# Kernel optimization log

Measured on AMD Instinct MI355X. Metric: run time of the kernel, lower is better.

The kernel has to match this reference:

```python
import jax, jax.numpy as jnp
import numpy as np

D_BINS = 16   # piecewise-linear bins
N_PROP = 10   # hard-coded in CountModule.__init__


def pwl(w, x):
    """PiecewiseLinear.forward: w is [D_BINS+1], x any shape in [0,1]."""
    aw = jnp.abs(w)
    nw = aw / aw.sum()
    cs = jnp.cumsum(nw)               # [17] cumulative knot values
    xd = x * D_BINS
    ip = jnp.floor(xd).astype(jnp.int32)   # x >= 0 so trunc == floor
    frac = xd - ip.astype(x.dtype)
    return cs[jnp.minimum(ip, D_BINS)] + frac * nw[jnp.minimum(ip + 1, D_BINS)]


def iou(a):
    """Pairwise IoU of boxes a [B,4,n] (coords y1,x1,y2,x2) -> [B,n,n]."""
    tl = jnp.maximum(a[:, :2, :, None], a[:, :2, None, :])  # [B,2,n,n]
    br = jnp.minimum(a[:, 2:, :, None], a[:, 2:, None, :])
    wh = jnp.clip(br - tl, 0.0)
    inter = wh[:, 0] * wh[:, 1]                               # [B,n,n]
    area = jnp.clip(a[:, 2] - a[:, 0], 0.0) * jnp.clip(a[:, 3] - a[:, 1], 0.0)  # [B,n]
    return inter / (area[:, :, None] + area[:, None, :] - inter + 1e-12)


def count_forward(boxes, attention, f_weights):
    n = N_PROP
    B = boxes.shape[0]
    f = lambda i, x: pwl(f_weights[i], x)
    # keep top-n proposals by attention score
    att_v, idx = jax.lax.top_k(attention, n)                  # [B,n]
    boxes_f = jnp.take_along_axis(
        boxes, jnp.broadcast_to(idx[:, None, :], (B, 4, n)), axis=2)  # [B,4,n]
    att = jax.nn.sigmoid(att_v)
    A = att[:, :, None] * att[:, None, :]                     # outer product [B,n,n]
    Dm = 1.0 - iou(boxes_f)                                   # [B,n,n]
    A_t = f(0, A) * f(1, Dm)
    X = f(3, A) * f(4, Dm)
    # deduplicate: outer_diff on 2D att gives pairwise |a_i - a_j|; on 3D X the
    # original torch code unsqueezes both operands at the same axis, yielding zeros
    att_diff = jnp.abs(att[:, :, None] - att[:, None, :])     # [B,n,n]
    xs = X[:, :, None, :]
    score_diff = jnp.broadcast_to(jnp.abs(xs - xs), (B, n, n, n))  # zeros, as in torch
    sim = f(2, 1.0 - att_diff) * jnp.prod(f(2, 1.0 - score_diff), axis=1)  # [B,n,n]
    s_i = sim.sum(axis=2)                                     # [B,n]
    s_st = s_i[:, :, None] * s_i[:, None, :]                  # [B,n,n]
    score = A_t / s_st
    corr = f(0, att * att) / s_i
    mod_E = score.sum(axis=(1, 2))[:, None] + corr.sum(axis=1, keepdims=True)  # [B,1]
    c = jnp.sqrt(mod_E + 1e-20)
    # to_k_hot: soft two-hot over counts 0..n
    cc = jnp.clip(c, 0.0, float(n))                           # [B,1]
    ip = jnp.floor(cc).astype(jnp.int32)
    frac = cc - ip.astype(cc.dtype)
    left = jax.nn.one_hot(jnp.minimum(ip[:, 0], n), n + 1, dtype=cc.dtype)
    right = jax.nn.one_hot(jnp.minimum(ip[:, 0] + 1, n), n + 1, dtype=cc.dtype)
    o = (1.0 - frac) * left + frac * right                    # [B,n+1]
    p_a = jnp.abs(f(5, att) - 0.5)                            # [B,n]
    p_d = jnp.abs(f(6, Dm) - 0.5)                             # [B,n,n]
    gate = f(7, p_a.mean(axis=1, keepdims=True)
             + p_d.mean(axis=2).mean(axis=1, keepdims=True))  # [B,1]
    return gate * o                                           # [B,n+1]


def setup_inputs() -> dict:
    key = jax.random.key(0)
    k1, k2, k3 = jax.random.split(key, 3)
    B, M = 32768, 36
    boxes = jax.random.uniform(k1, (B, 4, M), dtype=jnp.float32)
    attention = jax.random.normal(k2, (B, M), dtype=jnp.float32)
    f_weights = jax.random.uniform(k3, (8, D_BINS + 1), dtype=jnp.float32,
                                   minval=0.25, maxval=1.75)
    return {"boxes": boxes, "attention": attention, "f_weights": f_weights}


def reference(boxes, attention, f_weights):
    return count_forward(boxes, attention, f_weights)
```

## Files before the change

kernel.cpp:

```cpp
#include <hip/hip_runtime.h>
#include <cstdint>
#include <cstddef>

#define MM 36
#define NP 10
#define BLOCK 1024
#define GPB (BLOCK / 16)
#define WPB (BLOCK / 64)

template<int CTRL>
__device__ __forceinline__ float dpp_movf(float x) {
    return __int_as_float(__builtin_amdgcn_update_dpp(
        0, __float_as_int(x), CTRL, 0xF, 0xF, true));
}
__device__ __forceinline__ float rowmax16(float x) {
    x = fmaxf(x, dpp_movf<0xB1>(x));
    x = fmaxf(x, dpp_movf<0x4E>(x));
    x = fmaxf(x, dpp_movf<0x141>(x));
    x = fmaxf(x, dpp_movf<0x140>(x));
    return x;
}
__device__ __forceinline__ float rowsum16(float x) {
    x += dpp_movf<0xB1>(x);
    x += dpp_movf<0x4E>(x);
    x += dpp_movf<0x141>(x);
    x += dpp_movf<0x140>(x);
    return x;
}

__device__ __forceinline__ float pwl17(const float2* __restrict__ T, float x) {
    float xd = x * 16.0f;
    float fip = floorf(xd);
    float frac = xd - fip;
    int ip = (int)fminf(fip, 16.0f);
    float2 t = T[ip];
    return fmaf(frac, t.y, t.x);
}

__global__ __launch_bounds__(BLOCK) void count_kernel(
    const float* __restrict__ boxes,
    const float* __restrict__ attention,
    const float* __restrict__ fw,
    float* __restrict__ out,
    int B)
{
    __shared__ float2 Tw[WPB][4][17];
    __shared__ float4 T16w[WPB][17];
    __shared__ float  boxrow[GPB][4 * MM];
    __shared__ float4 propA[GPB][NP];
    __shared__ float2 propB[GPB][NP];
    __shared__ __align__(8) float invl[GPB][NP];

    const int tid  = threadIdx.x;
    const int lane = tid & 63;
    const int w    = tid >> 6;
    const int l    = tid & 15;
    const int g    = tid >> 4;
    int b = blockIdx.x * GPB + g;
    const bool valid = (b < B);
    b = valid ? b : (B - 1);

    const float* arow = attention + (size_t)b * MM;
    const float4* brow4 = reinterpret_cast<const float4*>(boxes + (size_t)b * (4 * MM));

    float v0 = arow[l];
    float v1 = arow[l + 16];
    float v2 = -INFINITY;
    if (l < 4) v2 = arow[l + 32];
    float4 B0 = brow4[l];
    float4 B1 = brow4[l + 16];
    float4 B2 = make_float4(0.f, 0.f, 0.f, 0.f);
    if (l < 4) B2 = brow4[l + 32];

    float4* bls = reinterpret_cast<float4*>(&boxrow[g][0]);
    bls[l] = B0;
    bls[l + 16] = B1;
    if (l < 4) bls[l + 32] = B2;

    if (lane < 8 && lane != 3 && lane != 4) {
        const float* wp = fw + lane * 17;
        float aw[17];
        float s = 0.f;
        #pragma unroll
        for (int k = 0; k < 17; ++k) { aw[k] = fabsf(wp[k]); s += aw[k]; }
        float is = __fdividef(1.0f, s);

        if (lane == 1 || lane == 6) {
            float* dst = &T16w[w][0].x + ((lane == 1) ? 0 : 2);
            float c = 0.f;
            #pragma unroll
            for (int k = 0; k < 17; ++k) {
                float nwk = aw[k] * is;
                c += nwk;
                dst[4 * k]     = c;
                dst[4 * k + 1] = ((k < 16) ? aw[k + 1] : aw[16]) * is;
            }
        } else {
            int row = (lane == 0) ? 0 : (lane == 2) ? 1 : (lane == 5) ? 2 : 3;
            float c = 0.f;
            #pragma unroll
            for (int k = 0; k < 17; ++k) {
                float nwk = aw[k] * is;
                c += nwk;
                Tw[w][row][k] = make_float2(c, ((k < 16) ? aw[k + 1] : aw[16]) * is);
            }
        }
    }

    const int gbase = tid & 48;
    int mi = 0; float mv = 0.f;
    #pragma unroll
    for (int t = 0; t < NP; ++t) {
        float vm = rowmax16(fmaxf(fmaxf(v0, v1), v2));
        unsigned long long b0 = __ballot(v0 == vm);
        unsigned long long b1 = __ballot(v1 == vm);
        unsigned long long b2 = __ballot(v2 == vm);
        unsigned g0 = (unsigned)(b0 >> gbase) & 0xFFFFu;
        unsigned g1 = (unsigned)(b1 >> gbase) & 0xFFFFu;
        unsigned g2 = (unsigned)(b2 >> gbase) & 0xFFFFu;
        int m = g0 ? (__ffs(g0) - 1)
              : (g1 ? (__ffs(g1) + 15)
                    : (__ffs(g2) + 31));
        if (l == t) { mi = m; mv = vm; }
        v0 = (m == l)      ? -INFINITY : v0;
        v1 = (m == l + 16) ? -INFINITY : v1;
        v2 = (m == l + 32) ? -INFINITY : v2;
    }

    float sattI = 0.f, y1I = 0.f, x1I = 0.f, y2I = 0.f, x2I = 0.f, areaI = 0.f;
    if (l < NP) {
        sattI = 1.0f / (1.0f + __expf(-mv));
        y1I = boxrow[g][mi];
        x1I = boxrow[g][mi + MM];
        y2I = boxrow[g][mi + 2 * MM];
        x2I = boxrow[g][mi + 3 * MM];
        areaI = fmaxf(y2I - y1I, 0.f) * fmaxf(x2I - x1I, 0.f);
        propA[g][l] = make_float4(y1I, x1I, y2I, x2I);
        propB[g][l] = make_float2(areaI, sattI);
    }

    const float2* T0 = &Tw[w][0][0];
    const float2* T2 = &Tw[w][1][0];
    const float2* T5 = &Tw[w][2][0];
    const float2* T7 = &Tw[w][3][0];
    const float4* T16 = &T16w[w][0];

    float cs2_16 = T2[16].x;
    float p2c = cs2_16 * cs2_16;
    float p4c = p2c * p2c;
    float p8c = p4c * p4c;
    float P = p8c * p2c;

    float at[NP];
    float s_um = 0.f, pdAcc = 0.f;
    #pragma unroll
    for (int j = 0; j < NP; ++j) {
        float4 pj = propA[g][j];
        float2 qj = propB[g][j];
        float ty = fmaxf(y1I, pj.x);
        float tx = fmaxf(x1I, pj.y);
        float by = fminf(y2I, pj.z);
        float bx = fminf(x2I, pj.w);
        float inter = fmaxf(by - ty, 0.f) * fmaxf(bx - tx, 0.f);
        float iouv = __fdividef(inter, areaI + qj.x - inter + 1e-12f);
        float Dm = fmaxf(1.0f - iouv, 0.0f);
        float A = sattI * qj.y;
        float xdD = Dm * 16.0f;
        float fipD = fminf(floorf(xdD), 16.0f);
        float frD = xdD - fipD;
        float4 t16 = T16[(int)fipD];
        float f1v = fmaf(frD, t16.y, t16.x);
        float f6v = fabsf(fmaf(frD, t16.w, t16.z) - 0.5f);
        at[j] = pwl17(T0, A) * f1v;
        s_um += pwl17(T2, 1.0f - fabsf(sattI - qj.y));
        pdAcc += f6v;
    }
    float s_i = s_um * P;

    float inv_i = 1.0f / s_i;
    if (l < NP) invl[g][l] = inv_i;

    float dot = 0.f;
    const float2* ivp = reinterpret_cast<const float2*>(&invl[g][0]);
    #pragma unroll
    for (int jj = 0; jj < NP / 2; ++jj) {
        float2 iv = ivp[jj];
        dot = fmaf(at[2 * jj], iv.x, dot);
        dot = fmaf(at[2 * jj + 1], iv.y, dot);
    }

    float corr = pwl17(T0, sattI * sattI) * inv_i;
    float fmask = (l < NP) ? 1.f : 0.f;
    float contrib = fmask * (inv_i * dot + corr);
    float pav = fmask * fabsf(pwl17(T5, sattI) - 0.5f);
    float pdv = fmask * pdAcc;

    contrib = rowsum16(contrib);
    pav = rowsum16(pav);
    pdv = rowsum16(pdv);

    float gate = pwl17(T7, pav * 0.1f + pdv * 0.01f);
    float cval = sqrtf(contrib + 1e-20f);
    cval = fminf(fmaxf(cval, 0.f), 10.0f);
    float fip = floorf(cval);
    int ipc = (int)fip;
    float frac = cval - fip;
    int i0 = ipc < 10 ? ipc : 10;
    int i1 = (ipc + 1) < 10 ? (ipc + 1) : 10;

    if (valid && l < NP + 1) {
        float val = ((l == i0) ? (1.0f - frac) * gate : 0.f)
                  + ((l == i1) ? frac * gate : 0.f);
        out[(size_t)b * (NP + 1) + l] = val;
    }
}

extern "C" void kernel_launch(void* const* d_in, const int* in_sizes, int n_in,
                              void* d_out, int out_size, void* d_ws, size_t ws_size,
                              hipStream_t stream) {
    const float* boxes = (const float*)d_in[0];
    const float* attention = (const float*)d_in[1];
    const float* fw = (const float*)d_in[2];
    float* out = (float*)d_out;
    int B = in_sizes[1] / MM;
    int grid = (B + GPB - 1) / GPB;
    hipLaunchKernelGGL(count_kernel, dim3(grid), dim3(BLOCK), 0, stream,
                       boxes, attention, fw, out, B);
}
```

Measured before the change: 27.03 us.

## Gather selected boxes directly from global memory and shrink block size

Removes the step that staged every proposal box row in shared memory. After top-k, only the 10 selected boxes are read straight from global memory, which cuts LDS use and store work but turns a coalesced vector load into scattered scalar gathers. The block size drops from 1024 to 256 threads. The inverse-s dot product now reads LDS with float4 loads, and the table-building branches are merged into one loop. Rows of `invl` are 40 bytes apart, so the 16-byte vector loads are not aligned for odd groups, which relies on the hardware tolerating unaligned LDS access.

```diff
diff --git a/kernel.cpp b/kernel.cpp
--- a/kernel.cpp
+++ b/kernel.cpp
@@ -4,7 +4,7 @@
 
 #define MM 36
 #define NP 10
-#define BLOCK 1024
+#define BLOCK 256
 #define GPB (BLOCK / 16)
 #define WPB (BLOCK / 64)
 
@@ -46,10 +46,9 @@
 {
     __shared__ float2 Tw[WPB][4][17];
     __shared__ float4 T16w[WPB][17];
-    __shared__ float  boxrow[GPB][4 * MM];
     __shared__ float4 propA[GPB][NP];
     __shared__ float2 propB[GPB][NP];
-    __shared__ __align__(8) float invl[GPB][NP];
+    __shared__ __align__(16) float invl[GPB][NP];
 
     const int tid  = threadIdx.x;
     const int lane = tid & 63;
@@ -61,21 +60,12 @@
     b = valid ? b : (B - 1);
 
     const float* arow = attention + (size_t)b * MM;
-    const float4* brow4 = reinterpret_cast<const float4*>(boxes + (size_t)b * (4 * MM));
+    const float* brow = boxes + (size_t)b * (4 * MM);
 
     float v0 = arow[l];
     float v1 = arow[l + 16];
     float v2 = -INFINITY;
     if (l < 4) v2 = arow[l + 32];
-    float4 B0 = brow4[l];
-    float4 B1 = brow4[l + 16];
-    float4 B2 = make_float4(0.f, 0.f, 0.f, 0.f);
-    if (l < 4) B2 = brow4[l + 32];
-
-    float4* bls = reinterpret_cast<float4*>(&boxrow[g][0]);
-    bls[l] = B0;
-    bls[l + 16] = B1;
-    if (l < 4) bls[l + 32] = B2;
 
     if (lane < 8 && lane != 3 && lane != 4) {
         const float* wp = fw + lane * 17;
@@ -85,25 +75,20 @@
         for (int k = 0; k < 17; ++k) { aw[k] = fabsf(wp[k]); s += aw[k]; }
         float is = __fdividef(1.0f, s);
 
-        if (lane == 1 || lane == 6) {
-            float* dst = &T16w[w][0].x + ((lane == 1) ? 0 : 2);
-            float c = 0.f;
-            #pragma unroll
-            for (int k = 0; k < 17; ++k) {
-                float nwk = aw[k] * is;
-                c += nwk;
-                dst[4 * k]     = c;
-                dst[4 * k + 1] = ((k < 16) ? aw[k + 1] : aw[16]) * is;
-            }
-        } else {
+        float2* base;
+        int str;
+        if (lane == 1)      { base = reinterpret_cast<float2*>(&T16w[w][0]);     str = 2; }
+        else if (lane == 6) { base = reinterpret_cast<float2*>(&T16w[w][0]) + 1; str = 2; }
+        else {
             int row = (lane == 0) ? 0 : (lane == 2) ? 1 : (lane == 5) ? 2 : 3;
-            float c = 0.f;
-            #pragma unroll
-            for (int k = 0; k < 17; ++k) {
-                float nwk = aw[k] * is;
-                c += nwk;
-                Tw[w][row][k] = make_float2(c, ((k < 16) ? aw[k + 1] : aw[16]) * is);
-            }
+            base = &Tw[w][row][0]; str = 1;
+        }
+        float c = 0.f;
+        #pragma unroll
+        for (int k = 0; k < 17; ++k) {
+            float nwk = aw[k] * is;
+            c += nwk;
+            base[k * str] = make_float2(c, ((k < 16) ? aw[k + 1] : aw[16]) * is);
         }
     }
 
@@ -130,10 +115,10 @@
     float sattI = 0.f, y1I = 0.f, x1I = 0.f, y2I = 0.f, x2I = 0.f, areaI = 0.f;
     if (l < NP) {
         sattI = 1.0f / (1.0f + __expf(-mv));
-        y1I = boxrow[g][mi];
-        x1I = boxrow[g][mi + MM];
-        y2I = boxrow[g][mi + 2 * MM];
-        x2I = boxrow[g][mi + 3 * MM];
+        y1I = brow[mi];
+        x1I = brow[mi + MM];
+        y2I = brow[mi + 2 * MM];
+        x2I = brow[mi + 3 * MM];
         areaI = fmaxf(y2I - y1I, 0.f) * fmaxf(x2I - x1I, 0.f);
         propA[g][l] = make_float4(y1I, x1I, y2I, x2I);
         propB[g][l] = make_float2(areaI, sattI);
@@ -180,14 +165,22 @@
     float inv_i = 1.0f / s_i;
     if (l < NP) invl[g][l] = inv_i;
 
+    const float4* f4p = reinterpret_cast<const float4*>(&invl[g][0]);
+    float4 ivA = f4p[0];
+    float4 ivB = f4p[1];
+    float2 ivC = *reinterpret_cast<const float2*>(&invl[g][8]);
+
     float dot = 0.f;
-    const float2* ivp = reinterpret_cast<const float2*>(&invl[g][0]);
-    #pragma unroll
-    for (int jj = 0; jj < NP / 2; ++jj) {
-        float2 iv = ivp[jj];
-        dot = fmaf(at[2 * jj], iv.x, dot);
-        dot = fmaf(at[2 * jj + 1], iv.y, dot);
-    }
+    dot = fmaf(at[0], ivA.x, dot);
+    dot = fmaf(at[1], ivA.y, dot);
+    dot = fmaf(at[2], ivA.z, dot);
+    dot = fmaf(at[3], ivA.w, dot);
+    dot = fmaf(at[4], ivB.x, dot);
+    dot = fmaf(at[5], ivB.y, dot);
+    dot = fmaf(at[6], ivB.z, dot);
+    dot = fmaf(at[7], ivB.w, dot);
+    dot = fmaf(at[8], ivC.x, dot);
+    dot = fmaf(at[9], ivC.y, dot);
 
     float corr = pwl17(T0, sattI * sattI) * inv_i;
     float fmask = (l < NP) ? 1.f : 0.f;
```

New measurement: 23.76 us. 12.1% less time.
